# Performance work log

Hardware: AMD Instinct MI355X
Metric: run time of the kernel (lower is better)

The kernel has to match this reference:

```python
import jax, jax.numpy as jnp
import numpy as np

D = 512  # hard-coded feature dim in the original module


def setup_inputs() -> dict:
    key = jax.random.key(0)
    x = jax.random.normal(key, (8, 8192, D), dtype=jnp.float32)
    return {"x": x}


def reference(x) -> jnp.ndarray:
    # Original: expectation_neg = ones_linear_neg(x) = -(sum over last dim),
    # broadcast to all 512 positions; forward returns x + expectation_neg
    # (everything after the first `return x` in the torch code is dead).
    # The variance/sqrt chain is computed in torch but unused by the output.
    neg_sum = -jnp.sum(x, axis=-1, keepdims=True)  # [..., 1], broadcasts over D
    return x + neg_sum
```

## Files before the change

### kernel.cpp

```cpp
#include <hip/hip_runtime.h>


#define D 512
#define WAVES_PER_BLOCK 4
#define BLOCK (WAVES_PER_BLOCK * 64)

typedef float v4f __attribute__((ext_vector_type(4)));

__global__ __launch_bounds__(BLOCK) void rowsub2_kernel(const float* __restrict__ x,
                                                        float* __restrict__ out,
                                                        int npairs) {
    const int wave = threadIdx.x >> 6;
    const int lane = threadIdx.x & 63;
    const long long pair = (long long)blockIdx.x * WAVES_PER_BLOCK + wave;
    if (pair >= npairs) return;

    const v4f* __restrict__ xr = reinterpret_cast<const v4f*>(x + pair * (2 * D));
    v4f* __restrict__ orow     = reinterpret_cast<v4f*>(out + pair * (2 * D));

    v4f a0 = __builtin_nontemporal_load(&xr[lane]);
    v4f a1 = __builtin_nontemporal_load(&xr[lane + 64]);
    v4f b0 = __builtin_nontemporal_load(&xr[lane + 128]);
    v4f b1 = __builtin_nontemporal_load(&xr[lane + 192]);

    float s0 = (a0.x + a0.y) + (a0.z + a0.w) + (a1.x + a1.y) + (a1.z + a1.w);
    float s1 = (b0.x + b0.y) + (b0.z + b0.w) + (b1.x + b1.y) + (b1.z + b1.w);

    #pragma unroll
    for (int off = 32; off > 0; off >>= 1) {
        s0 += __shfl_xor(s0, off, 64);
        s1 += __shfl_xor(s1, off, 64);
    }

    v4f ra0 = a0 - s0;
    v4f ra1 = a1 - s0;
    v4f rb0 = b0 - s1;
    v4f rb1 = b1 - s1;

    __builtin_nontemporal_store(ra0, &orow[lane]);
    __builtin_nontemporal_store(ra1, &orow[lane + 64]);
    __builtin_nontemporal_store(rb0, &orow[lane + 128]);
    __builtin_nontemporal_store(rb1, &orow[lane + 192]);
}

extern "C" void kernel_launch(void* const* d_in, const int* in_sizes, int n_in,
                              void* d_out, int out_size, void* d_ws, size_t ws_size,
                              hipStream_t stream) {
    const float* x = (const float*)d_in[0];
    float* out = (float*)d_out;
    const int nrows = in_sizes[0] / D;
    const int npairs = nrows / 2;
    const int grid = (npairs + WAVES_PER_BLOCK - 1) / WAVES_PER_BLOCK;
    rowsub2_kernel<<<grid, BLOCK, 0, stream>>>(x, out, npairs);
}
```

Before: 217.6 us.

## Use persistent grid-stride waves with register double-buffered row prefetch

Replaces one-pair-per-wave launch with a fixed 2048-block grid where each wave loops over row pairs with a grid stride. The next pair's loads are issued before reducing and storing the current pair, overlapping memory latency with the shuffle reduction and stores. This adds register pressure from holding two pairs and fixes the grid size, which may affect occupancy and load balance.

```diff
diff --git a/kernel.cpp b/kernel.cpp
--- a/kernel.cpp
+++ b/kernel.cpp
@@ -2,45 +2,60 @@
 
 
 #define D 512
-#define WAVES_PER_BLOCK 4
-#define BLOCK (WAVES_PER_BLOCK * 64)
+#define BLOCK 256
+#define WPB (BLOCK / 64)
 
 typedef float v4f __attribute__((ext_vector_type(4)));
 
-__global__ __launch_bounds__(BLOCK) void rowsub2_kernel(const float* __restrict__ x,
-                                                        float* __restrict__ out,
-                                                        int npairs) {
-    const int wave = threadIdx.x >> 6;
-    const int lane = threadIdx.x & 63;
-    const long long pair = (long long)blockIdx.x * WAVES_PER_BLOCK + wave;
-    if (pair >= npairs) return;
+__global__ __launch_bounds__(BLOCK) void rowsub_pipe_kernel(const float* __restrict__ x,
+                                                            float* __restrict__ out,
+                                                            int npairs) {
+    const int lane  = threadIdx.x & 63;
+    const int gwave = blockIdx.x * WPB + (threadIdx.x >> 6);
+    const int nwaves = gridDim.x * WPB;
 
-    const v4f* __restrict__ xr = reinterpret_cast<const v4f*>(x + pair * (2 * D));
-    v4f* __restrict__ orow     = reinterpret_cast<v4f*>(out + pair * (2 * D));
+    long long p = gwave;
+    if (p >= npairs) return;
 
+    const v4f* __restrict__ xb = reinterpret_cast<const v4f*>(x);
+    v4f* __restrict__ ob       = reinterpret_cast<v4f*>(out);
+
+    const v4f* xr = xb + p * 256;
     v4f a0 = __builtin_nontemporal_load(&xr[lane]);
     v4f a1 = __builtin_nontemporal_load(&xr[lane + 64]);
     v4f b0 = __builtin_nontemporal_load(&xr[lane + 128]);
     v4f b1 = __builtin_nontemporal_load(&xr[lane + 192]);
 
-    float s0 = (a0.x + a0.y) + (a0.z + a0.w) + (a1.x + a1.y) + (a1.z + a1.w);
-    float s1 = (b0.x + b0.y) + (b0.z + b0.w) + (b1.x + b1.y) + (b1.z + b1.w);
+    while (true) {
+        const long long pn = p + nwaves;
+        const bool more = (pn < npairs);
+        v4f c0, c1, e0, e1;
+        if (more) {
+            const v4f* xn = xb + pn * 256;
+            c0 = __builtin_nontemporal_load(&xn[lane]);
+            c1 = __builtin_nontemporal_load(&xn[lane + 64]);
+            e0 = __builtin_nontemporal_load(&xn[lane + 128]);
+            e1 = __builtin_nontemporal_load(&xn[lane + 192]);
+        }
 
-    #pragma unroll
-    for (int off = 32; off > 0; off >>= 1) {
-        s0 += __shfl_xor(s0, off, 64);
-        s1 += __shfl_xor(s1, off, 64);
+        float s0 = (a0.x + a0.y) + (a0.z + a0.w) + (a1.x + a1.y) + (a1.z + a1.w);
+        float s1 = (b0.x + b0.y) + (b0.z + b0.w) + (b1.x + b1.y) + (b1.z + b1.w);
+        #pragma unroll
+        for (int off = 32; off > 0; off >>= 1) {
+            s0 += __shfl_xor(s0, off, 64);
+            s1 += __shfl_xor(s1, off, 64);
+        }
+
+        v4f* orow = ob + p * 256;
+        __builtin_nontemporal_store(a0 - s0, &orow[lane]);
+        __builtin_nontemporal_store(a1 - s0, &orow[lane + 64]);
+        __builtin_nontemporal_store(b0 - s1, &orow[lane + 128]);
+        __builtin_nontemporal_store(b1 - s1, &orow[lane + 192]);
+
+        if (!more) break;
+        a0 = c0; a1 = c1; b0 = e0; b1 = e1;
+        p = pn;
     }
-
-    v4f ra0 = a0 - s0;
-    v4f ra1 = a1 - s0;
-    v4f rb0 = b0 - s1;
-    v4f rb1 = b1 - s1;
-
-    __builtin_nontemporal_store(ra0, &orow[lane]);
-    __builtin_nontemporal_store(ra1, &orow[lane + 64]);
-    __builtin_nontemporal_store(rb0, &orow[lane + 128]);
-    __builtin_nontemporal_store(rb1, &orow[lane + 192]);
 }
 
 extern "C" void kernel_launch(void* const* d_in, const int* in_sizes, int n_in,
@@ -48,8 +63,8 @@
                               hipStream_t stream) {
     const float* x = (const float*)d_in[0];
     float* out = (float*)d_out;
-    const int nrows = in_sizes[0] / D;
+    const int nrows  = in_sizes[0] / D;
     const int npairs = nrows / 2;
-    const int grid = (npairs + WAVES_PER_BLOCK - 1) / WAVES_PER_BLOCK;
-    rowsub2_kernel<<<grid, BLOCK, 0, stream>>>(x, out, npairs);
+    const int grid = 2048;
+    rowsub_pipe_kernel<<<grid, BLOCK, 0, stream>>>(x, out, npairs);
 }
```

After: 218.4 us. Within noise of the previous version (+0.3%).
